# Optimization experiments

Measured on AMD Instinct MI355X. Metric: run time of the kernel, lower is better.

## Reference

```python
import jax, jax.numpy as jnp
import numpy as np

B, N, M, NS = 4, 32768, 1024, 32
RADIUS = 0.1
EPS = 1e-5
CHANS = [16, 32, 32, 64]


def setup_inputs() -> dict:
    key = jax.random.key(0)
    ks = jax.random.split(key, 8)
    d = {
        'theta': jax.random.uniform(ks[0], (B, N), jnp.float32, 0.0, float(np.pi)),
        'phi': jax.random.uniform(ks[1], (B, N), jnp.float32, 0.0, 2.0 * float(np.pi)),
        'features': jax.random.normal(ks[2], (B, CHANS[0], N), jnp.float32),
    }
    for i, (ci, co) in enumerate(zip(CHANS[:-1], CHANS[1:])):
        d[f'w{i}'] = jax.random.normal(jax.random.fold_in(ks[3], i), (co, ci), jnp.float32) * 0.1
        d[f'b{i}'] = jnp.zeros((co,), jnp.float32)
        d[f'g{i}'] = jnp.ones((co,), jnp.float32)
        d[f'be{i}'] = jnp.zeros((co,), jnp.float32)
    return d


def _group(theta, phi, features):
    # angular ball query + random neighbor sampling (deterministic key),
    # duplicates padded with the first valid neighbor (max-pool invariant,
    # matching the torch code's sampling-with-replacement semantics).
    k1, k2 = jax.random.split(jax.random.key(42))
    n = theta.shape[1]
    cent_idx = jax.random.permutation(k1, n)[:M]                 # shared across batch, like torch code
    ct = theta[:, cent_idx]                                      # (B, M)
    cp = phi[:, cent_idx]
    th_s, ph_s = jax.lax.stop_gradient(theta), jax.lax.stop_gradient(phi)
    ct_s, cp_s = jax.lax.stop_gradient(ct), jax.lax.stop_gradient(cp)
    dist = jnp.sqrt((th_s[:, None, :] - ct_s[:, :, None]) ** 2 +
                    (ph_s[:, None, :] - cp_s[:, :, None]) ** 2)  # (B, M, N)
    mask = dist <= RADIUS
    scores = jnp.where(mask, jax.random.uniform(k2, dist.shape, jnp.float32), jnp.inf)
    _, idx = jax.lax.top_k(-scores, NS)                          # NS random in-ball indices, (B, M, NS)
    valid = jnp.take_along_axis(mask, idx, axis=-1)
    idx = jnp.where(valid, idx, idx[..., :1])                    # centroid itself is always valid at slot 0
    gathered = jax.vmap(lambda f, i: f[:, i])(features, idx)     # (B, C, M, NS)
    grouped = jnp.transpose(gathered, (0, 1, 3, 2))              # (B, C, NS, M)
    return ct, cp, grouped


def _mlp_max(x, params):
    # 1x1 conv + BatchNorm (batch stats, training mode) + ReLU stack, then max over nsample
    for w, b, g, be in params:
        x = jnp.einsum('oc,bcsm->bosm', w, x) + b[None, :, None, None]
        mu = x.mean(axis=(0, 2, 3), keepdims=True)
        var = x.var(axis=(0, 2, 3), keepdims=True)
        x = (x - mu) * jax.lax.rsqrt(var + EPS) * g[None, :, None, None] + be[None, :, None, None]
        x = jax.nn.relu(x)
    return x.max(axis=2)                                         # (B, C_out, M)


def reference(theta, phi, features, w0, b0, g0, be0, w1, b1, g1, be1, w2, b2, g2, be2):
    params = [(w0, b0, g0, be0), (w1, b1, g1, be1), (w2, b2, g2, be2)]
    ct, cp, grouped = _group(theta, phi, features)
    new_feats = _mlp_max(grouped, params)
    return ct, cp, new_feats
```

## Files before the change

### kernel.cpp

```cpp
#include <hip/hip_runtime.h>
#include <stdint.h>

#define N_PTS 32768
#define M_CENT 1024
#define B_SZ 4
#define NS 32
#define NR 64
#define P_TOT (B_SZ * NS * M_CENT)

#define GT 29
#define GP 58
#define NCELL (GT * GP)
#define INVF (1.0f / 0.11f)
#define CAPW 320

__device__ __forceinline__ int cell_t(float t) {
  return min(GT - 1, (int)(t * INVF));
}
__device__ __forceinline__ int cell_p(float p) {
  return min(GP - 1, (int)(p * INVF));
}

struct Key2 { uint32_t a, b; };

__device__ __forceinline__ uint32_t rotl32(uint32_t v, uint32_t r) {
  return (v << r) | (v >> (32u - r));
}

__device__ __forceinline__ void tf2x32(uint32_t k0, uint32_t k1,
                                       uint32_t& x0, uint32_t& x1) {
  uint32_t ks0 = k0, ks1 = k1, ks2 = k0 ^ k1 ^ 0x1BD11BDAu;
  x0 += ks0; x1 += ks1;
#define TF_ROUND(r) { x0 += x1; x1 = rotl32(x1, r); x1 ^= x0; }
  TF_ROUND(13u) TF_ROUND(15u) TF_ROUND(26u) TF_ROUND(6u)
  x0 += ks1; x1 += ks2 + 1u;
  TF_ROUND(17u) TF_ROUND(29u) TF_ROUND(16u) TF_ROUND(24u)
  x0 += ks2; x1 += ks0 + 2u;
  TF_ROUND(13u) TF_ROUND(15u) TF_ROUND(26u) TF_ROUND(6u)
  x0 += ks0; x1 += ks1 + 3u;
  TF_ROUND(17u) TF_ROUND(29u) TF_ROUND(16u) TF_ROUND(24u)
  x0 += ks1; x1 += ks2 + 4u;
  TF_ROUND(13u) TF_ROUND(15u) TF_ROUND(26u) TF_ROUND(6u)
  x0 += ks2; x1 += ks0 + 5u;
#undef TF_ROUND
}

__device__ __forceinline__ Key2 tf_block(Key2 k, uint32_t hi, uint32_t lo) {
  uint32_t x0 = hi, x1 = lo;
  tf2x32(k.a, k.b, x0, x1);
  Key2 r; r.a = x0; r.b = x1; return r;
}

__global__ __launch_bounds__(256) void perm_bits_kernel(uint32_t* __restrict__ bits1,
                                                        uint32_t* __restrict__ bits2) {
  int j = blockIdx.x * 256 + threadIdx.x;
  Key2 root; root.a = 0u; root.b = 42u;
  Key2 k1   = tf_block(root, 0u, 0u);
  Key2 keyA = tf_block(k1, 0u, 0u);
  Key2 sub1 = tf_block(k1, 0u, 1u);
  Key2 sub2 = tf_block(keyA, 0u, 1u);
  Key2 r1 = tf_block(sub1, 0u, (uint32_t)j);
  Key2 r2 = tf_block(sub2, 0u, (uint32_t)j);
  bits1[j] = r1.a ^ r1.b;
  bits2[j] = r2.a ^ r2.b;
}

__global__ __launch_bounds__(256) void hist_kernel(const uint32_t* __restrict__ bits1,
                                                   const uint32_t* __restrict__ bits2,
                                                   int* __restrict__ hist1,
                                                   int* __restrict__ hist2) {
  int j = blockIdx.x * 256 + threadIdx.x;
  atomicAdd(&hist1[bits1[j] >> 16], 1);
  atomicAdd(&hist2[bits2[j] >> 16], 1);
}

__global__ __launch_bounds__(256) void gsum_scan_kernel(const int* __restrict__ hist1,
                                                        const int* __restrict__ hist2,
                                                        int* __restrict__ gbase1,
                                                        int* __restrict__ gbase2) {
  __shared__ int s[256];
  const int* hist = blockIdx.x == 0 ? hist1 : hist2;
  int* gbase = blockIdx.x == 0 ? gbase1 : gbase2;
  int g = threadIdx.x;
  int sum = 0;
  for (int i = 0; i < 256; ++i) sum += hist[g * 256 + i];
  s[g] = sum;
  __syncthreads();
  if (g == 0) {
    int run = 0;
    for (int i = 0; i < 256; ++i) { int t = s[i]; s[i] = run; run += t; }
  }
  __syncthreads();
  gbase[g] = s[g];
}

__global__ __launch_bounds__(256) void bucket_scan_kernel(const int* __restrict__ hist1,
                                                          const int* __restrict__ hist2,
                                                          const int* __restrict__ gbase1,
                                                          const int* __restrict__ gbase2,
                                                          int* __restrict__ prefix1,
                                                          int* __restrict__ prefix2,
                                                          int* __restrict__ cursor1,
                                                          int* __restrict__ cursor2) {
  __shared__ int s[256];
  const int* hist = blockIdx.y == 0 ? hist1 : hist2;
  const int* gbase = blockIdx.y == 0 ? gbase1 : gbase2;
  int* prefix = blockIdx.y == 0 ? prefix1 : prefix2;
  int* cursor = blockIdx.y == 0 ? cursor1 : cursor2;
  int g = blockIdx.x, t = threadIdx.x;
  int idx = g * 256 + t;
  int orig = hist[idx];
  s[t] = orig;
  __syncthreads();
  for (int off = 1; off < 256; off <<= 1) {
    int v = (t >= off) ? s[t - off] : 0;
    __syncthreads();
    s[t] += v;
    __syncthreads();
  }
  int pref = gbase[g] + s[t] - orig;
  prefix[idx] = pref;
  cursor[idx] = pref;
}

__global__ __launch_bounds__(256) void bucket_scatter_kernel(const uint32_t* __restrict__ bits1,
                                                             const uint32_t* __restrict__ bits2,
                                                             int* __restrict__ cursor1,
                                                             int* __restrict__ cursor2,
                                                             int* __restrict__ sorted1,
                                                             int* __restrict__ sorted2) {
  int j = blockIdx.x * 256 + threadIdx.x;
  int p1 = atomicAdd(&cursor1[bits1[j] >> 16], 1);
  sorted1[p1] = j;
  int p2 = atomicAdd(&cursor2[bits2[j] >> 16], 1);
  sorted2[p2] = j;
}

__device__ __forceinline__ int exact_rank(const uint32_t* __restrict__ bits,
                                          const int* __restrict__ prefix,
                                          const int* __restrict__ hist,
                                          const int* __restrict__ sorted, int j) {
  uint32_t my = bits[j];
  int b = (int)(my >> 16);
  int start = prefix[b];
  int cnt = hist[b];
  int r = start;
  for (int i = 0; i < cnt; ++i) {
    int m = sorted[start + i];
    uint32_t vb = bits[m];
    if (vb < my || (vb == my && m < j)) ++r;
  }
  return r;
}

__global__ __launch_bounds__(256) void rank_scatter1_kernel(
    const uint32_t* __restrict__ bits1, const uint32_t* __restrict__ bits2,
    const int* __restrict__ prefix1, const int* __restrict__ prefix2,
    const int* __restrict__ hist1, const int* __restrict__ hist2,
    const int* __restrict__ sorted1, const int* __restrict__ sorted2,
    int* __restrict__ xmid, int* __restrict__ rank2) {
  int j = blockIdx.x * 256 + threadIdx.x;
  int r1 = exact_rank(bits1, prefix1, hist1, sorted1, j);
  xmid[r1] = j;
  rank2[j] = exact_rank(bits2, prefix2, hist2, sorted2, j);
}

__global__ __launch_bounds__(256) void scatter2_kernel(const int* __restrict__ rank2,
                                                       const int* __restrict__ xmid,
                                                       int* __restrict__ xfin) {
  int p = blockIdx.x * 256 + threadIdx.x;
  xfin[rank2[p]] = xmid[p];
}

__global__ __launch_bounds__(256) void cell_hist_kernel(const float* __restrict__ theta,
                                                        const float* __restrict__ phi,
                                                        int* __restrict__ cellcnt) {
  int j = blockIdx.x * 256 + threadIdx.x;
  int b = j >> 15;
  atomicAdd(&cellcnt[b * NCELL + cell_t(theta[j]) * GP + cell_p(phi[j])], 1);
}

__global__ __launch_bounds__(256) void cell_scan_kernel(const int* __restrict__ cellcnt,
                                                        int* __restrict__ cellpre,
                                                        int* __restrict__ cellcur) {
  __shared__ int s[256];
  int b = blockIdx.x, t = threadIdx.x;
  const int* cnt = cellcnt + b * NCELL;
  int i0 = t * 7, i1 = min(i0 + 7, NCELL);
  int sum = 0;
  for (int i = i0; i < i1; ++i) sum += cnt[i];
  s[t] = sum;
  __syncthreads();
  for (int off = 1; off < 256; off <<= 1) {
    int v = (t >= off) ? s[t - off] : 0;
    __syncthreads();
    s[t] += v;
    __syncthreads();
  }
  int run = (t == 0) ? 0 : s[t - 1];
  for (int i = i0; i < i1; ++i) {
    cellpre[b * NCELL + i] = run;
    cellcur[b * NCELL + i] = run;
    run += cnt[i];
  }
}

__global__ __launch_bounds__(256) void cell_scatter_kernel(const float* __restrict__ theta,
                                                           const float* __restrict__ phi,
                                                           int* __restrict__ cellcur,
                                                           float* __restrict__ px,
                                                           float* __restrict__ py,
                                                           int* __restrict__ pid) {
  int j = blockIdx.x * 256 + threadIdx.x;
  int b = j >> 15, n = j & (N_PTS - 1);
  float t = theta[j], p = phi[j];
  int cell = b * NCELL + cell_t(t) * GP + cell_p(p);
  int pos = atomicAdd(&cellcur[cell], 1);
  px[(b << 15) + pos] = t;
  py[(b << 15) + pos] = p;
  pid[(b << 15) + pos] = n;
}

__global__ __launch_bounds__(256) void select_kernel(
    const float* __restrict__ theta, const float* __restrict__ phi,
    const int* __restrict__ cent,
    const int* __restrict__ cellpre, const int* __restrict__ cellcnt,
    const float* __restrict__ px, const float* __restrict__ py,
    const int* __restrict__ pid,
    int* __restrict__ idx_buf, float* __restrict__ out_ct, float* __restrict__ out_cp) {
  __shared__ float wsc[4][CAPW];
  __shared__ int wsn[4][CAPW];
  int tid = threadIdx.x;
  int w = tid >> 6, lane = tid & 63;
  int bm = blockIdx.x * 4 + w;
  int b = bm >> 10, m = bm & 1023;
  int ci = cent[m];
  float ctv = theta[(b << 15) + ci];
  float cpv = phi[(b << 15) + ci];
  if (lane == 0) { out_ct[bm] = ctv; out_cp[bm] = cpv; }

  Key2 root; root.a = 0u; root.b = 42u;
  Key2 k2 = tf_block(root, 0u, 1u);
  uint32_t flat_base = (uint32_t)bm << 15;

  int tc = cell_t(ctv), pc = cell_p(cpv);
  int t0 = max(0, tc - 1), t1 = min(GT - 1, tc + 1);
  int p0 = max(0, pc - 1), p1 = min(GP - 1, pc + 1);

  const float* bpx = px + ((size_t)b << 15);
  const float* bpy = py + ((size_t)b << 15);
  const int* bpid = pid + ((size_t)b << 15);
  int wcnt = 0;
  for (int tcell = t0; tcell <= t1; ++tcell) {
    for (int pcell = p0; pcell <= p1; ++pcell) {
      int cell = b * NCELL + tcell * GP + pcell;
      int start = cellpre[cell];
      int cnt = cellcnt[cell];
      for (int base = 0; base < cnt; base += 64) {
        int i = base + lane;
        bool hit = false; float sc = 0.0f; int n = 0;
        if (i < cnt) {
          float t = bpx[start + i], p = bpy[start + i];
          float dx = __fsub_rn(t, ctv);
          float dy = __fsub_rn(p, cpv);
          float d = __fsqrt_rn(__fadd_rn(__fmul_rn(dx, dx), __fmul_rn(dy, dy)));
          if (d <= 0.1f) {
            hit = true; n = bpid[start + i];
            Key2 r = tf_block(k2, 0u, flat_base + (uint32_t)n);
            uint32_t bits = r.a ^ r.b;
            sc = __uint_as_float(0x3f800000u | (bits >> 9)) - 1.0f;
          }
        }
        unsigned long long mask = __ballot(hit);
        int pos = wcnt + __popcll(mask & ((1ull << lane) - 1ull));
        if (hit && pos < CAPW) { wsc[w][pos] = sc; wsn[w][pos] = n; }
        wcnt = min(wcnt + (int)__popcll(mask), CAPW);
      }
    }
  }
  __syncthreads();

  float ls = -1.0f; int ln = -1;
  int sel0 = -1, mysel = -1;
  for (int r = 0; r < NS; ++r) {
    float best = 3.0e38f; int bn = 0x7fffffff;
    for (int i = lane; i < wcnt; i += 64) {
      float s = wsc[w][i]; int n = wsn[w][i];
      bool after = (s > ls) || (s == ls && n > ln);
      bool better = (s < best) || (s == best && n < bn);
      if (after && better) { best = s; bn = n; }
    }
    for (int off = 32; off; off >>= 1) {
      float os = __shfl_xor(best, off);
      int on = __shfl_xor(bn, off);
      if (os < best || (os == best && on < bn)) { best = os; bn = on; }
    }
    int chosen;
    if (best < 3.0e38f) { ls = best; ln = bn; chosen = bn; }
    else chosen = sel0;
    if (r == 0) sel0 = chosen;
    if (lane == r) mysel = chosen;
  }
  if (lane < NS) idx_buf[bm * NS + lane] = mysel;
}

__device__ __forceinline__ float bn_relu(float y, float mu, float r, float g, float be) {
  float t = __fsub_rn(y, mu);
  t = __fmul_rn(t, r);
  t = __fmul_rn(t, g);
  t = __fadd_rn(t, be);
  return fmaxf(t, 0.0f);
}

template <int CO>
__device__ __forceinline__ void accum_stats_pad(const float* __restrict__ Yp,
                                                double* __restrict__ S, int tid, int bid) {
  if (tid < CO) {
    double s1 = 0.0, s2 = 0.0;
#pragma unroll
    for (int s = 0; s < NS; ++s) {
      double v = (double)Yp[tid * 33 + s];
      s1 += v; s2 += v * v;
    }
    double* base = S + (size_t)(bid & (NR - 1)) * (2 * CO);
    atomicAdd(base + tid, s1);
    atomicAdd(base + CO + tid, s2);
  }
}

__global__ __launch_bounds__(256) void pass1_kernel(
    const float* __restrict__ feat, const int* __restrict__ idx_buf,
    const float* __restrict__ w0, const float* __restrict__ b0,
    float* __restrict__ stash, double* __restrict__ stats, int mode) {
  __shared__ int idxs[NS];
  __shared__ float X1[512];
  __shared__ float Yp[32 * 33];
  int bm = blockIdx.x, tid = threadIdx.x, b = bm >> 10;
  if (tid < NS) idxs[tid] = idx_buf[bm * NS + tid];
  __syncthreads();
  for (int v = tid; v < 512; v += 256) {
    int c = v >> 5, s = v & 31;
    float val = feat[(size_t)(b * 16 + c) * N_PTS + idxs[s]];
    X1[v] = val;
    if (mode == 1) stash[(size_t)bm * 512 + v] = val;
  }
  __syncthreads();
  for (int v = tid; v < 1024; v += 256) {
    int o = v >> 5, s = v & 31;
    float acc = b0[o];
#pragma unroll
    for (int c = 0; c < 16; ++c) acc = fmaf(w0[o * 16 + c], X1[c * 32 + s], acc);
    Yp[o * 33 + s] = acc;
    if (mode == 2) stash[(size_t)bm * 1024 + v] = acc;
  }
  __syncthreads();
  accum_stats_pad<32>(Yp, stats, tid, bm);
}

__global__ __launch_bounds__(256) void pass2s_kernel(
    const float* __restrict__ Y1g,
    const float* __restrict__ mur1, const float* __restrict__ g0, const float* __restrict__ be0,
    const float* __restrict__ w1, const float* __restrict__ b1,
    float* __restrict__ Y2g, double* __restrict__ stats) {
  __shared__ float X2[1024];
  __shared__ float Yp[32 * 33];
  int bm = blockIdx.x, tid = threadIdx.x;
  for (int v = tid; v < 1024; v += 256) {
    int o = v >> 5;
    X2[v] = bn_relu(Y1g[(size_t)bm * 1024 + v], mur1[o], mur1[32 + o], g0[o], be0[o]);
  }
  __syncthreads();
  for (int v = tid; v < 1024; v += 256) {
    int o = v >> 5, s = v & 31;
    float acc = b1[o];
#pragma unroll
    for (int c = 0; c < 32; ++c) acc = fmaf(w1[o * 32 + c], X2[c * 32 + s], acc);
    Yp[o * 33 + s] = acc;
    Y2g[(size_t)bm * 1024 + v] = acc;
  }
  __syncthreads();
  accum_stats_pad<32>(Yp, stats, tid, bm);
}

__global__ __launch_bounds__(256) void pass3s_kernel(
    const float* __restrict__ Y2g,
    const float* __restrict__ mur2, const float* __restrict__ g1, const float* __restrict__ be1,
    const float* __restrict__ w2, const float* __restrict__ b2,
    float* __restrict__ mm3, double* __restrict__ stats) {
  __shared__ float X3[1024];
  __shared__ float Yp[64 * 33];
  int bm = blockIdx.x, tid = threadIdx.x;
  for (int v = tid; v < 1024; v += 256) {
    int o = v >> 5;
    X3[v] = bn_relu(Y2g[(size_t)bm * 1024 + v], mur2[o], mur2[32 + o], g1[o], be1[o]);
  }
  __syncthreads();
  for (int v = tid; v < 2048; v += 256) {
    int o = v >> 5, s = v & 31;
    float acc = b2[o];
#pragma unroll
    for (int c = 0; c < 32; ++c) acc = fmaf(w2[o * 32 + c], X3[c * 32 + s], acc);
    Yp[o * 33 + s] = acc;
  }
  __syncthreads();
  if (tid < 64) {
    double s1 = 0.0, s2 = 0.0;
    float mx = -3.0e38f, mn = 3.0e38f;
#pragma unroll
    for (int s = 0; s < NS; ++s) {
      float y = Yp[tid * 33 + s];
      double v = (double)y;
      s1 += v; s2 += v * v;
      mx = fmaxf(mx, y); mn = fminf(mn, y);
    }
    double* base = stats + (size_t)(bm & (NR - 1)) * 128;
    atomicAdd(base + tid, s1);
    atomicAdd(base + 64 + tid, s2);
    mm3[bm * 128 + tid * 2] = mx;
    mm3[bm * 128 + tid * 2 + 1] = mn;
  }
}

__global__ __launch_bounds__(256) void final_small_kernel(
    const float* __restrict__ mm3,
    const float* __restrict__ mur3, const float* __restrict__ g2, const float* __restrict__ be2,
    float* __restrict__ out_ft) {
  int j = blockIdx.x * 256 + threadIdx.x;
  int b = j >> 16, o = (j >> 10) & 63, m = j & 1023;
  int bm = b * 1024 + m;
  float g = g2[o];
  float y = (g >= 0.0f) ? mm3[bm * 128 + o * 2] : mm3[bm * 128 + o * 2 + 1];
  out_ft[j] = bn_relu(y, mur3[o], mur3[64 + o], g, be2[o]);
}

__device__ __forceinline__ void load_x1(int big, const float* __restrict__ X1g,
                                        const float* __restrict__ feat,
                                        const int* __restrict__ idx_buf,
                                        int bm, int b, int tid,
                                        int* idxs, float* X1) {
  if (!big) {
    if (tid < NS) idxs[tid] = idx_buf[bm * NS + tid];
  }
  __syncthreads();
  if (big) {
    for (int v = tid; v < 512; v += 256) X1[v] = X1g[(size_t)bm * 512 + v];
  } else {
    for (int v = tid; v < 512; v += 256) {
      int c = v >> 5, s = v & 31;
      X1[v] = feat[(size_t)(b * 16 + c) * N_PTS + idxs[s]];
    }
  }
}

__global__ __launch_bounds__(256) void pass2_rec_kernel(
    const float* __restrict__ X1g, const float* __restrict__ feat,
    const int* __restrict__ idx_buf,
    const float* __restrict__ w0, const float* __restrict__ b0,
    const float* __restrict__ mur1, const float* __restrict__ g0, const float* __restrict__ be0,
    const float* __restrict__ w1, const float* __restrict__ b1,
    double* __restrict__ stats, int big) {
  __shared__ int idxs[NS];
  __shared__ float X1[512];
  __shared__ float X2[1024];
  __shared__ float Yp[32 * 33];
  int bm = blockIdx.x, tid = threadIdx.x, b = bm >> 10;
  load_x1(big, X1g, feat, idx_buf, bm, b, tid, idxs, X1);
  __syncthreads();
  for (int v = tid; v < 1024; v += 256) {
    int o = v >> 5, s = v & 31;
    float acc = b0[o];
#pragma unroll
    for (int c = 0; c < 16; ++c) acc = fmaf(w0[o * 16 + c], X1[c * 32 + s], acc);
    X2[v] = bn_relu(acc, mur1[o], mur1[32 + o], g0[o], be0[o]);
  }
  __syncthreads();
  for (int v = tid; v < 1024; v += 256) {
    int o = v >> 5, s = v & 31;
    float acc = b1[o];
#pragma unroll
    for (int c = 0; c < 32; ++c) acc = fmaf(w1[o * 32 + c], X2[c * 32 + s], acc);
    Yp[o * 33 + s] = acc;
  }
  __syncthreads();
  accum_stats_pad<32>(Yp, stats, tid, bm);
}

__global__ __launch_bounds__(256) void pass3_rec_kernel(
    const float* __restrict__ X1g, const float* __restrict__ feat,
    const int* __restrict__ idx_buf,
    const float* __restrict__ w0, const float* __restrict__ b0,
    const float* __restrict__ mur1, const float* __restrict__ g0, const float* __restrict__ be0,
    const float* __restrict__ w1, const float* __restrict__ b1,
    const float* __restrict__ mur2, const float* __restrict__ g1, const float* __restrict__ be1,
    const float* __restrict__ w2, const float* __restrict__ b2,
    float* __restrict__ mm3, double* __restrict__ stats, int big) {
  __shared__ int idxs[NS];
  __shared__ float X1[512];
  __shared__ float X2[1024];
  __shared__ float X3[1024];
  __shared__ float Yp[64 * 33];
  int bm = blockIdx.x, tid = threadIdx.x, b = bm >> 10;
  load_x1(big, X1g, feat, idx_buf, bm, b, tid, idxs, X1);
  __syncthreads();
  for (int v = tid; v < 1024; v += 256) {
    int o = v >> 5, s = v & 31;
    float acc = b0[o];
#pragma unroll
    for (int c = 0; c < 16; ++c) acc = fmaf(w0[o * 16 + c], X1[c * 32 + s], acc);
    X2[v] = bn_relu(acc, mur1[o], mur1[32 + o], g0[o], be0[o]);
  }
  __syncthreads();
  for (int v = tid; v < 1024; v += 256) {
    int o = v >> 5, s = v & 31;
    float acc = b1[o];
#pragma unroll
    for (int c = 0; c < 32; ++c) acc = fmaf(w1[o * 32 + c], X2[c * 32 + s], acc);
    X3[v] = bn_relu(acc, mur2[o], mur2[32 + o], g1[o], be1[o]);
  }
  __syncthreads();
  for (int v = tid; v < 2048; v += 256) {
    int o = v >> 5, s = v & 31;
    float acc = b2[o];
#pragma unroll
    for (int c = 0; c < 32; ++c) acc = fmaf(w2[o * 32 + c], X3[c * 32 + s], acc);
    Yp[o * 33 + s] = acc;
  }
  __syncthreads();
  if (tid < 64) {
    double s1 = 0.0, s2 = 0.0;
    float mx = -3.0e38f, mn = 3.0e38f;
#pragma unroll
    for (int s = 0; s < NS; ++s) {
      float y = Yp[tid * 33 + s];
      double v = (double)y;
      s1 += v; s2 += v * v;
      mx = fmaxf(mx, y); mn = fminf(mn, y);
    }
    double* base = stats + (size_t)(bm & (NR - 1)) * 128;
    atomicAdd(base + tid, s1);
    atomicAdd(base + 64 + tid, s2);
    mm3[bm * 128 + tid * 2] = mx;
    mm3[bm * 128 + tid * 2 + 1] = mn;
  }
}

template <int CO>
__global__ void fixup_mur_kernel(const double* __restrict__ S, float* __restrict__ mur) {
  int o = threadIdx.x;
  if (o >= CO) return;
  double s1 = 0.0, s2 = 0.0;
  for (int r = 0; r < NR; ++r) {
    s1 += S[r * 2 * CO + o];
    s2 += S[r * 2 * CO + CO + o];
  }
  const double P = (double)P_TOT;
  double mu = s1 / P;
  double var = s2 / P - mu * mu;
  mur[o] = (float)mu;
  mur[CO + o] = (float)(1.0 / sqrt(var + 1e-5));
}

extern "C" void kernel_launch(void* const* d_in, const int* in_sizes, int n_in,
                              void* d_out, int out_size, void* d_ws, size_t ws_size,
                              hipStream_t stream) {
  (void)in_sizes; (void)n_in; (void)out_size;
  const float* theta = (const float*)d_in[0];
  const float* phi   = (const float*)d_in[1];
  const float* feat  = (const float*)d_in[2];
  const float* w0 = (const float*)d_in[3];
  const float* b0 = (const float*)d_in[4];
  const float* g0 = (const float*)d_in[5];
  const float* be0 = (const float*)d_in[6];
  const float* w1 = (const float*)d_in[7];
  const float* b1 = (const float*)d_in[8];
  const float* g1 = (const float*)d_in[9];
  const float* be1 = (const float*)d_in[10];
  const float* w2 = (const float*)d_in[11];
  const float* b2 = (const float*)d_in[12];
  const float* g2 = (const float*)d_in[13];
  const float* be2 = (const float*)d_in[14];

  float* out = (float*)d_out;
  float* out_ct = out;
  float* out_cp = out + B_SZ * M_CENT;
  float* out_ft = out + 2 * B_SZ * M_CENT;

  char* ws = (char*)d_ws;
  uint32_t* bits1 = (uint32_t*)(ws + 0);
  uint32_t* bits2 = (uint32_t*)(ws + 131072);
  int* rank2 = (int*)(ws + 262144);
  int* xmid  = (int*)(ws + 393216);
  int* xfin  = (int*)(ws + 524288);
  int* idx_buf = (int*)(ws + 655360);
  int* hist1   = (int*)(ws + 1179648);
  int* hist2   = (int*)(ws + 1441792);
  int* prefix1 = (int*)(ws + 1703936);
  int* prefix2 = (int*)(ws + 1966080);
  int* cursor1 = (int*)(ws + 2228224);
  int* cursor2 = (int*)(ws + 2490368);
  int* sorted1 = (int*)(ws + 2752512);
  int* sorted2 = (int*)(ws + 2883584);
  int* gbase1  = (int*)(ws + 3014656);
  int* gbase2  = (int*)(ws + 3015680);
  int* cellcnt = (int*)(ws + 3016704);
  int* cellpre = (int*)(ws + 3049472);
  int* cellcur = (int*)(ws + 3082240);
  float* px    = (float*)(ws + 3115008);
  float* py    = (float*)(ws + 3639296);
  int* pid     = (int*)(ws + 4163584);
  double* stats1 = (double*)(ws + 4687872);
  double* stats2 = (double*)(ws + 4720640);
  double* stats3 = (double*)(ws + 4753408);
  float* mur1 = (float*)(ws + 4818944);
  float* mur2 = (float*)(ws + 4819200);
  float* mur3 = (float*)(ws + 4819456);
  float* mm3  = (float*)(ws + 4820480);
  float* stash = (float*)(ws + 6917632);
  float* Y2g  = (float*)(ws + 23694848);
  size_t NEED_FULL = (size_t)40472064;
  size_t NEED_BIG  = (size_t)6917632 + 8388608;
  int full = (ws_size >= NEED_FULL) ? 1 : 0;
  int big  = (!full && ws_size >= NEED_BIG) ? 1 : 0;

  hipMemsetAsync(hist1, 0, 524288, stream);
  hipMemsetAsync(cellcnt, 0, 32768, stream);
  hipMemsetAsync(stats1, 0, 131072, stream);

  perm_bits_kernel<<<128, 256, 0, stream>>>(bits1, bits2);
  hist_kernel<<<128, 256, 0, stream>>>(bits1, bits2, hist1, hist2);
  gsum_scan_kernel<<<2, 256, 0, stream>>>(hist1, hist2, gbase1, gbase2);
  bucket_scan_kernel<<<dim3(256, 2), 256, 0, stream>>>(hist1, hist2, gbase1, gbase2,
                                                       prefix1, prefix2, cursor1, cursor2);
  bucket_scatter_kernel<<<128, 256, 0, stream>>>(bits1, bits2, cursor1, cursor2,
                                                 sorted1, sorted2);
  rank_scatter1_kernel<<<128, 256, 0, stream>>>(bits1, bits2, prefix1, prefix2,
                                                hist1, hist2, sorted1, sorted2,
                                                xmid, rank2);
  scatter2_kernel<<<128, 256, 0, stream>>>(rank2, xmid, xfin);

  cell_hist_kernel<<<512, 256, 0, stream>>>(theta, phi, cellcnt);
  cell_scan_kernel<<<4, 256, 0, stream>>>(cellcnt, cellpre, cellcur);
  cell_scatter_kernel<<<512, 256, 0, stream>>>(theta, phi, cellcur, px, py, pid);

  select_kernel<<<1024, 256, 0, stream>>>(theta, phi, xfin, cellpre, cellcnt,
                                          px, py, pid, idx_buf, out_ct, out_cp);

  int mode = full ? 2 : (big ? 1 : 0);
  pass1_kernel<<<4096, 256, 0, stream>>>(feat, idx_buf, w0, b0, stash, stats1, mode);
  fixup_mur_kernel<32><<<1, 64, 0, stream>>>(stats1, mur1);
  if (full) {
    pass2s_kernel<<<4096, 256, 0, stream>>>(stash, mur1, g0, be0, w1, b1, Y2g, stats2);
    fixup_mur_kernel<32><<<1, 64, 0, stream>>>(stats2, mur2);
    pass3s_kernel<<<4096, 256, 0, stream>>>(Y2g, mur2, g1, be1, w2, b2, mm3, stats3);
  } else {
    pass2_rec_kernel<<<4096, 256, 0, stream>>>(stash, feat, idx_buf, w0, b0, mur1, g0, be0,
                                               w1, b1, stats2, big);
    fixup_mur_kernel<32><<<1, 64, 0, stream>>>(stats2, mur2);
    pass3_rec_kernel<<<4096, 256, 0, stream>>>(stash, feat, idx_buf, w0, b0, mur1, g0, be0,
                                               w1, b1, mur2, g1, be1, w2, b2, mm3, stats3, big);
  }
  fixup_mur_kernel<64><<<1, 64, 0, stream>>>(stats3, mur3);
  final_small_kernel<<<1024, 256, 0, stream>>>(mm3, mur3, g2, be2, out_ft);
}
```

Before: 289.0 us.

## Fuse preprocessing kernels, pack points as float4, transpose features, recompute layer-2 activations

Merges the permutation-bit, histogram and cell-count kernels into one prep kernel, and merges the two scans and the two scatters, which cuts launches. Points are stored as packed float4 so each load brings theta, phi and id together. The select kernel walks the 3x3 neighbour cells as one flattened range and uses a bitonic sort when there are at most 64 hits. A transposed feature copy lets pass1 gather each point with float4 loads. The Y2 stash is dropped: pass3 recomputes layer-2 from the Y1 stash, trading extra FLOPs for less memory traffic and a smaller workspace.

Result: faster. 277.0 us (-4.2%).

```diff
diff --git a/kernel.cpp b/kernel.cpp
--- a/kernel.cpp
+++ b/kernel.cpp
@@ -51,47 +51,96 @@
   Key2 r; r.a = x0; r.b = x1; return r;
 }
 
-__global__ __launch_bounds__(256) void perm_bits_kernel(uint32_t* __restrict__ bits1,
-                                                        uint32_t* __restrict__ bits2) {
+__global__ __launch_bounds__(256) void prep_kernel(const float* __restrict__ theta,
+                                                   const float* __restrict__ phi,
+                                                   uint32_t* __restrict__ bits1,
+                                                   uint32_t* __restrict__ bits2,
+                                                   int* __restrict__ hist1,
+                                                   int* __restrict__ hist2,
+                                                   int* __restrict__ cellcnt) {
   int j = blockIdx.x * 256 + threadIdx.x;
-  Key2 root; root.a = 0u; root.b = 42u;
-  Key2 k1   = tf_block(root, 0u, 0u);
-  Key2 keyA = tf_block(k1, 0u, 0u);
-  Key2 sub1 = tf_block(k1, 0u, 1u);
-  Key2 sub2 = tf_block(keyA, 0u, 1u);
-  Key2 r1 = tf_block(sub1, 0u, (uint32_t)j);
-  Key2 r2 = tf_block(sub2, 0u, (uint32_t)j);
-  bits1[j] = r1.a ^ r1.b;
-  bits2[j] = r2.a ^ r2.b;
-}
-
-__global__ __launch_bounds__(256) void hist_kernel(const uint32_t* __restrict__ bits1,
-                                                   const uint32_t* __restrict__ bits2,
-                                                   int* __restrict__ hist1,
-                                                   int* __restrict__ hist2) {
-  int j = blockIdx.x * 256 + threadIdx.x;
-  atomicAdd(&hist1[bits1[j] >> 16], 1);
-  atomicAdd(&hist2[bits2[j] >> 16], 1);
-}
-
-__global__ __launch_bounds__(256) void gsum_scan_kernel(const int* __restrict__ hist1,
-                                                        const int* __restrict__ hist2,
-                                                        int* __restrict__ gbase1,
-                                                        int* __restrict__ gbase2) {
+  int b = j >> 15;
+  float t = theta[j], p = phi[j];
+  atomicAdd(&cellcnt[b * NCELL + cell_t(t) * GP + cell_p(p)], 1);
+  if (j < N_PTS) {
+    Key2 root; root.a = 0u; root.b = 42u;
+    Key2 k1   = tf_block(root, 0u, 0u);
+    Key2 keyA = tf_block(k1, 0u, 0u);
+    Key2 sub1 = tf_block(k1, 0u, 1u);
+    Key2 sub2 = tf_block(keyA, 0u, 1u);
+    Key2 r1 = tf_block(sub1, 0u, (uint32_t)j);
+    Key2 r2 = tf_block(sub2, 0u, (uint32_t)j);
+    uint32_t v1 = r1.a ^ r1.b, v2 = r2.a ^ r2.b;
+    bits1[j] = v1; bits2[j] = v2;
+    atomicAdd(&hist1[v1 >> 16], 1);
+    atomicAdd(&hist2[v2 >> 16], 1);
+  }
+}
+
+__global__ __launch_bounds__(256) void transpose_kernel(const float* __restrict__ feat,
+                                                        float* __restrict__ featT) {
+  __shared__ float lds[16][65];
+  int b = blockIdx.y;
+  int n0 = blockIdx.x * 64;
+  int tid = threadIdx.x;
+#pragma unroll
+  for (int k = 0; k < 4; ++k) {
+    int v = tid + k * 256;
+    int c = v >> 6, no = v & 63;
+    lds[c][no] = feat[((size_t)(b * 16 + c) << 15) + n0 + no];
+  }
+  __syncthreads();
+#pragma unroll
+  for (int k = 0; k < 4; ++k) {
+    int v = tid + k * 256;
+    int no = v >> 4, c = v & 15;
+    featT[((size_t)(b << 15) + n0 + no) * 16 + c] = lds[c][no];
+  }
+}
+
+__global__ __launch_bounds__(256) void scans_kernel(const int* __restrict__ hist1,
+                                                    const int* __restrict__ hist2,
+                                                    int* __restrict__ gbase1,
+                                                    int* __restrict__ gbase2,
+                                                    const int* __restrict__ cellcnt,
+                                                    int* __restrict__ cellpre,
+                                                    int* __restrict__ cellcur) {
   __shared__ int s[256];
-  const int* hist = blockIdx.x == 0 ? hist1 : hist2;
-  int* gbase = blockIdx.x == 0 ? gbase1 : gbase2;
-  int g = threadIdx.x;
-  int sum = 0;
-  for (int i = 0; i < 256; ++i) sum += hist[g * 256 + i];
-  s[g] = sum;
-  __syncthreads();
-  if (g == 0) {
-    int run = 0;
-    for (int i = 0; i < 256; ++i) { int t = s[i]; s[i] = run; run += t; }
-  }
-  __syncthreads();
-  gbase[g] = s[g];
+  int t = threadIdx.x;
+  if (blockIdx.x < 2) {
+    const int* hist = blockIdx.x == 0 ? hist1 : hist2;
+    int* gbase = blockIdx.x == 0 ? gbase1 : gbase2;
+    int sum = 0;
+    for (int i = 0; i < 256; ++i) sum += hist[t * 256 + i];
+    s[t] = sum;
+    __syncthreads();
+    if (t == 0) {
+      int run = 0;
+      for (int i = 0; i < 256; ++i) { int v = s[i]; s[i] = run; run += v; }
+    }
+    __syncthreads();
+    gbase[t] = s[t];
+  } else {
+    int b = blockIdx.x - 2;
+    const int* cnt = cellcnt + b * NCELL;
+    int i0 = t * 7, i1 = min(i0 + 7, NCELL);
+    int sum = 0;
+    for (int i = i0; i < i1; ++i) sum += cnt[i];
+    s[t] = sum;
+    __syncthreads();
+    for (int off = 1; off < 256; off <<= 1) {
+      int v = (t >= off) ? s[t - off] : 0;
+      __syncthreads();
+      s[t] += v;
+      __syncthreads();
+    }
+    int run = (t == 0) ? 0 : s[t - 1];
+    for (int i = i0; i < i1; ++i) {
+      cellpre[b * NCELL + i] = run;
+      cellcur[b * NCELL + i] = run;
+      run += cnt[i];
+    }
+  }
 }
 
 __global__ __launch_bounds__(256) void bucket_scan_kernel(const int* __restrict__ hist1,
@@ -123,17 +172,28 @@
   cursor[idx] = pref;
 }
 
-__global__ __launch_bounds__(256) void bucket_scatter_kernel(const uint32_t* __restrict__ bits1,
-                                                             const uint32_t* __restrict__ bits2,
-                                                             int* __restrict__ cursor1,
-                                                             int* __restrict__ cursor2,
-                                                             int* __restrict__ sorted1,
-                                                             int* __restrict__ sorted2) {
+__global__ __launch_bounds__(256) void scatter_kernel(const float* __restrict__ theta,
+                                                      const float* __restrict__ phi,
+                                                      int* __restrict__ cellcur,
+                                                      float4* __restrict__ pts4,
+                                                      const uint32_t* __restrict__ bits1,
+                                                      const uint32_t* __restrict__ bits2,
+                                                      int* __restrict__ cursor1,
+                                                      int* __restrict__ cursor2,
+                                                      int* __restrict__ sorted1,
+                                                      int* __restrict__ sorted2) {
   int j = blockIdx.x * 256 + threadIdx.x;
-  int p1 = atomicAdd(&cursor1[bits1[j] >> 16], 1);
-  sorted1[p1] = j;
-  int p2 = atomicAdd(&cursor2[bits2[j] >> 16], 1);
-  sorted2[p2] = j;
+  int b = j >> 15, n = j & (N_PTS - 1);
+  float t = theta[j], p = phi[j];
+  int cell = b * NCELL + cell_t(t) * GP + cell_p(p);
+  int pos = atomicAdd(&cellcur[cell], 1);
+  pts4[(b << 15) + pos] = make_float4(t, p, __int_as_float(n), 0.0f);
+  if (j < N_PTS) {
+    int p1 = atomicAdd(&cursor1[bits1[j] >> 16], 1);
+    sorted1[p1] = j;
+    int p2 = atomicAdd(&cursor2[bits2[j] >> 16], 1);
+    sorted2[p2] = j;
+  }
 }
 
 __device__ __forceinline__ int exact_rank(const uint32_t* __restrict__ bits,
@@ -172,61 +232,11 @@
   xfin[rank2[p]] = xmid[p];
 }
 
-__global__ __launch_bounds__(256) void cell_hist_kernel(const float* __restrict__ theta,
-                                                        const float* __restrict__ phi,
-                                                        int* __restrict__ cellcnt) {
-  int j = blockIdx.x * 256 + threadIdx.x;
-  int b = j >> 15;
-  atomicAdd(&cellcnt[b * NCELL + cell_t(theta[j]) * GP + cell_p(phi[j])], 1);
-}
-
-__global__ __launch_bounds__(256) void cell_scan_kernel(const int* __restrict__ cellcnt,
-                                                        int* __restrict__ cellpre,
-                                                        int* __restrict__ cellcur) {
-  __shared__ int s[256];
-  int b = blockIdx.x, t = threadIdx.x;
-  const int* cnt = cellcnt + b * NCELL;
-  int i0 = t * 7, i1 = min(i0 + 7, NCELL);
-  int sum = 0;
-  for (int i = i0; i < i1; ++i) sum += cnt[i];
-  s[t] = sum;
-  __syncthreads();
-  for (int off = 1; off < 256; off <<= 1) {
-    int v = (t >= off) ? s[t - off] : 0;
-    __syncthreads();
-    s[t] += v;
-    __syncthreads();
-  }
-  int run = (t == 0) ? 0 : s[t - 1];
-  for (int i = i0; i < i1; ++i) {
-    cellpre[b * NCELL + i] = run;
-    cellcur[b * NCELL + i] = run;
-    run += cnt[i];
-  }
-}
-
-__global__ __launch_bounds__(256) void cell_scatter_kernel(const float* __restrict__ theta,
-                                                           const float* __restrict__ phi,
-                                                           int* __restrict__ cellcur,
-                                                           float* __restrict__ px,
-                                                           float* __restrict__ py,
-                                                           int* __restrict__ pid) {
-  int j = blockIdx.x * 256 + threadIdx.x;
-  int b = j >> 15, n = j & (N_PTS - 1);
-  float t = theta[j], p = phi[j];
-  int cell = b * NCELL + cell_t(t) * GP + cell_p(p);
-  int pos = atomicAdd(&cellcur[cell], 1);
-  px[(b << 15) + pos] = t;
-  py[(b << 15) + pos] = p;
-  pid[(b << 15) + pos] = n;
-}
-
 __global__ __launch_bounds__(256) void select_kernel(
     const float* __restrict__ theta, const float* __restrict__ phi,
     const int* __restrict__ cent,
     const int* __restrict__ cellpre, const int* __restrict__ cellcnt,
-    const float* __restrict__ px, const float* __restrict__ py,
-    const int* __restrict__ pid,
+    const float4* __restrict__ pts4,
     int* __restrict__ idx_buf, float* __restrict__ out_ct, float* __restrict__ out_cp) {
   __shared__ float wsc[4][CAPW];
   __shared__ int wsn[4][CAPW];
@@ -246,60 +256,95 @@
   int tc = cell_t(ctv), pc = cell_p(cpv);
   int t0 = max(0, tc - 1), t1 = min(GT - 1, tc + 1);
   int p0 = max(0, pc - 1), p1 = min(GP - 1, pc + 1);
-
-  const float* bpx = px + ((size_t)b << 15);
-  const float* bpy = py + ((size_t)b << 15);
-  const int* bpid = pid + ((size_t)b << 15);
+  int nct = t1 - t0 + 1, ncp = p1 - p0 + 1, ncells = nct * ncp;
+
+  int cst = 0, ccn = 0;
+  if (lane < ncells) {
+    int cell = b * NCELL + (t0 + lane / ncp) * GP + (p0 + lane % ncp);
+    cst = cellpre[cell];
+    ccn = cellcnt[cell];
+  }
+  int sc9[9], cc9[9];
+#pragma unroll
+  for (int k = 0; k < 9; ++k) {
+    sc9[k] = __shfl(cst, k);
+    cc9[k] = __shfl(ccn, k);
+  }
+  int T = 0;
+#pragma unroll
+  for (int k = 0; k < 9; ++k) T += cc9[k];
+
+  const float4* bpts = pts4 + ((size_t)b << 15);
   int wcnt = 0;
-  for (int tcell = t0; tcell <= t1; ++tcell) {
-    for (int pcell = p0; pcell <= p1; ++pcell) {
-      int cell = b * NCELL + tcell * GP + pcell;
-      int start = cellpre[cell];
-      int cnt = cellcnt[cell];
-      for (int base = 0; base < cnt; base += 64) {
-        int i = base + lane;
-        bool hit = false; float sc = 0.0f; int n = 0;
-        if (i < cnt) {
-          float t = bpx[start + i], p = bpy[start + i];
-          float dx = __fsub_rn(t, ctv);
-          float dy = __fsub_rn(p, cpv);
-          float d = __fsqrt_rn(__fadd_rn(__fmul_rn(dx, dx), __fmul_rn(dy, dy)));
-          if (d <= 0.1f) {
-            hit = true; n = bpid[start + i];
-            Key2 r = tf_block(k2, 0u, flat_base + (uint32_t)n);
-            uint32_t bits = r.a ^ r.b;
-            sc = __uint_as_float(0x3f800000u | (bits >> 9)) - 1.0f;
-          }
-        }
-        unsigned long long mask = __ballot(hit);
-        int pos = wcnt + __popcll(mask & ((1ull << lane) - 1ull));
-        if (hit && pos < CAPW) { wsc[w][pos] = sc; wsn[w][pos] = n; }
-        wcnt = min(wcnt + (int)__popcll(mask), CAPW);
+  for (int base = 0; base < T; base += 64) {
+    int i = base + lane;
+    bool hit = false; float sc = 0.0f; int n = 0;
+    if (i < T) {
+      int gidx = 0, acc = 0;
+#pragma unroll
+      for (int k = 0; k < 9; ++k) {
+        int lo = acc; acc += cc9[k];
+        if (i >= lo && i < acc) gidx = sc9[k] + (i - lo);
       }
-    }
-  }
-  __syncthreads();
-
-  float ls = -1.0f; int ln = -1;
-  int sel0 = -1, mysel = -1;
-  for (int r = 0; r < NS; ++r) {
-    float best = 3.0e38f; int bn = 0x7fffffff;
-    for (int i = lane; i < wcnt; i += 64) {
-      float s = wsc[w][i]; int n = wsn[w][i];
-      bool after = (s > ls) || (s == ls && n > ln);
-      bool better = (s < best) || (s == best && n < bn);
-      if (after && better) { best = s; bn = n; }
-    }
-    for (int off = 32; off; off >>= 1) {
-      float os = __shfl_xor(best, off);
-      int on = __shfl_xor(bn, off);
-      if (os < best || (os == best && on < bn)) { best = os; bn = on; }
-    }
-    int chosen;
-    if (best < 3.0e38f) { ls = best; ln = bn; chosen = bn; }
-    else chosen = sel0;
-    if (r == 0) sel0 = chosen;
-    if (lane == r) mysel = chosen;
+      float4 pt = bpts[gidx];
+      float dx = __fsub_rn(pt.x, ctv);
+      float dy = __fsub_rn(pt.y, cpv);
+      float d = __fsqrt_rn(__fadd_rn(__fmul_rn(dx, dx), __fmul_rn(dy, dy)));
+      if (d <= 0.1f) {
+        hit = true; n = __float_as_int(pt.z);
+        Key2 r = tf_block(k2, 0u, flat_base + (uint32_t)n);
+        uint32_t bits = r.a ^ r.b;
+        sc = __uint_as_float(0x3f800000u | (bits >> 9)) - 1.0f;
+      }
+    }
+    unsigned long long mask = __ballot(hit);
+    int pos = wcnt + __popcll(mask & ((1ull << lane) - 1ull));
+    if (hit && pos < CAPW) { wsc[w][pos] = sc; wsn[w][pos] = n; }
+    wcnt = min(wcnt + (int)__popcll(mask), CAPW);
+  }
+
+  int mysel;
+  if (wcnt <= 64) {
+    float s = (lane < wcnt) ? wsc[w][lane] : 3.0e38f;
+    int n = (lane < wcnt) ? wsn[w][lane] : 0x7fffffff;
+#pragma unroll
+    for (int k = 2; k <= 64; k <<= 1) {
+#pragma unroll
+      for (int jj = k >> 1; jj > 0; jj >>= 1) {
+        float os = __shfl_xor(s, jj);
+        int on = __shfl_xor(n, jj);
+        bool lower = (lane & jj) == 0;
+        bool dir = (lane & k) == 0;
+        bool mineFirst = (s < os) || (s == os && n < on);
+        bool takeMine = ((lower == mineFirst) == dir);
+        s = takeMine ? s : os;
+        n = takeMine ? n : on;
+      }
+    }
+    int n0 = __shfl(n, 0);
+    mysel = (lane < wcnt) ? n : n0;
+  } else {
+    float ls = -1.0f; int ln = -1;
+    int sel0 = -1; mysel = -1;
+    for (int r = 0; r < NS; ++r) {
+      float best = 3.0e38f; int bn = 0x7fffffff;
+      for (int i = lane; i < wcnt; i += 64) {
+        float s = wsc[w][i]; int n = wsn[w][i];
+        bool after = (s > ls) || (s == ls && n > ln);
+        bool better = (s < best) || (s == best && n < bn);
+        if (after && better) { best = s; bn = n; }
+      }
+      for (int off = 32; off; off >>= 1) {
+        float os = __shfl_xor(best, off);
+        int on = __shfl_xor(bn, off);
+        if (os < best || (os == best && on < bn)) { best = os; bn = on; }
+      }
+      int chosen;
+      if (best < 3.0e38f) { ls = best; ln = bn; chosen = bn; }
+      else chosen = sel0;
+      if (r == 0) sel0 = chosen;
+      if (lane == r) mysel = chosen;
+    }
   }
   if (lane < NS) idx_buf[bm * NS + lane] = mysel;
 }
@@ -329,7 +374,8 @@
 }
 
 __global__ __launch_bounds__(256) void pass1_kernel(
-    const float* __restrict__ feat, const int* __restrict__ idx_buf,
+    const float* __restrict__ feat, const float* __restrict__ featT,
+    const int* __restrict__ idx_buf,
     const float* __restrict__ w0, const float* __restrict__ b0,
     float* __restrict__ stash, double* __restrict__ stats, int mode) {
   __shared__ int idxs[NS];
@@ -338,11 +384,23 @@
   int bm = blockIdx.x, tid = threadIdx.x, b = bm >> 10;
   if (tid < NS) idxs[tid] = idx_buf[bm * NS + tid];
   __syncthreads();
-  for (int v = tid; v < 512; v += 256) {
-    int c = v >> 5, s = v & 31;
-    float val = feat[(size_t)(b * 16 + c) * N_PTS + idxs[s]];
-    X1[v] = val;
-    if (mode == 1) stash[(size_t)bm * 512 + v] = val;
+  if (mode == 3) {
+    if (tid < 128) {
+      int s = tid >> 2, c4 = tid & 3;
+      float4 f = *reinterpret_cast<const float4*>(
+          &featT[((size_t)(b << 15) + idxs[s]) * 16 + c4 * 4]);
+      X1[(c4 * 4 + 0) * 32 + s] = f.x;
+      X1[(c4 * 4 + 1) * 32 + s] = f.y;
+      X1[(c4 * 4 + 2) * 32 + s] = f.z;
+      X1[(c4 * 4 + 3) * 32 + s] = f.w;
+    }
+  } else {
+    for (int v = tid; v < 512; v += 256) {
+      int c = v >> 5, s = v & 31;
+      float val = feat[(size_t)(b * 16 + c) * N_PTS + idxs[s]];
+      X1[v] = val;
+      if (mode == 1) stash[(size_t)bm * 512 + v] = val;
+    }
   }
   __syncthreads();
   for (int v = tid; v < 1024; v += 256) {
@@ -351,7 +409,7 @@
 #pragma unroll
     for (int c = 0; c < 16; ++c) acc = fmaf(w0[o * 16 + c], X1[c * 32 + s], acc);
     Yp[o * 33 + s] = acc;
-    if (mode == 2) stash[(size_t)bm * 1024 + v] = acc;
+    if (mode >= 2) stash[(size_t)bm * 1024 + v] = acc;
   }
   __syncthreads();
   accum_stats_pad<32>(Yp, stats, tid, bm);
@@ -361,7 +419,7 @@
     const float* __restrict__ Y1g,
     const float* __restrict__ mur1, const float* __restrict__ g0, const float* __restrict__ be0,
     const float* __restrict__ w1, const float* __restrict__ b1,
-    float* __restrict__ Y2g, double* __restrict__ stats) {
+    double* __restrict__ stats) {
   __shared__ float X2[1024];
   __shared__ float Yp[32 * 33];
   int bm = blockIdx.x, tid = threadIdx.x;
@@ -376,23 +434,33 @@
 #pragma unroll
     for (int c = 0; c < 32; ++c) acc = fmaf(w1[o * 32 + c], X2[c * 32 + s], acc);
     Yp[o * 33 + s] = acc;
-    Y2g[(size_t)bm * 1024 + v] = acc;
   }
   __syncthreads();
   accum_stats_pad<32>(Yp, stats, tid, bm);
 }
 
 __global__ __launch_bounds__(256) void pass3s_kernel(
-    const float* __restrict__ Y2g,
+    const float* __restrict__ Y1g,
+    const float* __restrict__ mur1, const float* __restrict__ g0, const float* __restrict__ be0,
+    const float* __restrict__ w1, const float* __restrict__ b1,
     const float* __restrict__ mur2, const float* __restrict__ g1, const float* __restrict__ be1,
     const float* __restrict__ w2, const float* __restrict__ b2,
     float* __restrict__ mm3, double* __restrict__ stats) {
+  __shared__ float X2[1024];
   __shared__ float X3[1024];
   __shared__ float Yp[64 * 33];
   int bm = blockIdx.x, tid = threadIdx.x;
   for (int v = tid; v < 1024; v += 256) {
     int o = v >> 5;
-    X3[v] = bn_relu(Y2g[(size_t)bm * 1024 + v], mur2[o], mur2[32 + o], g1[o], be1[o]);
+    X2[v] = bn_relu(Y1g[(size_t)bm * 1024 + v], mur1[o], mur1[32 + o], g0[o], be0[o]);
+  }
+  __syncthreads();
+  for (int v = tid; v < 1024; v += 256) {
+    int o = v >> 5, s = v & 31;
+    float acc = b1[o];
+#pragma unroll
+    for (int c = 0; c < 32; ++c) acc = fmaf(w1[o * 32 + c], X2[c * 32 + s], acc);
+    X3[v] = bn_relu(acc, mur2[o], mur2[32 + o], g1[o], be1[o]);
   }
   __syncthreads();
   for (int v = tid; v < 2048; v += 256) {
@@ -594,70 +662,67 @@
   int* idx_buf = (int*)(ws + 655360);
   int* hist1   = (int*)(ws + 1179648);
   int* hist2   = (int*)(ws + 1441792);
-  int* prefix1 = (int*)(ws + 1703936);
-  int* prefix2 = (int*)(ws + 1966080);
-  int* cursor1 = (int*)(ws + 2228224);
-  int* cursor2 = (int*)(ws + 2490368);
-  int* sorted1 = (int*)(ws + 2752512);
-  int* sorted2 = (int*)(ws + 2883584);
-  int* gbase1  = (int*)(ws + 3014656);
-  int* gbase2  = (int*)(ws + 3015680);
-  int* cellcnt = (int*)(ws + 3016704);
-  int* cellpre = (int*)(ws + 3049472);
-  int* cellcur = (int*)(ws + 3082240);
-  float* px    = (float*)(ws + 3115008);
-  float* py    = (float*)(ws + 3639296);
-  int* pid     = (int*)(ws + 4163584);
-  double* stats1 = (double*)(ws + 4687872);
-  double* stats2 = (double*)(ws + 4720640);
-  double* stats3 = (double*)(ws + 4753408);
-  float* mur1 = (float*)(ws + 4818944);
-  float* mur2 = (float*)(ws + 4819200);
-  float* mur3 = (float*)(ws + 4819456);
-  float* mm3  = (float*)(ws + 4820480);
-  float* stash = (float*)(ws + 6917632);
-  float* Y2g  = (float*)(ws + 23694848);
-  size_t NEED_FULL = (size_t)40472064;
-  size_t NEED_BIG  = (size_t)6917632 + 8388608;
-  int full = (ws_size >= NEED_FULL) ? 1 : 0;
-  int big  = (!full && ws_size >= NEED_BIG) ? 1 : 0;
-
-  hipMemsetAsync(hist1, 0, 524288, stream);
-  hipMemsetAsync(cellcnt, 0, 32768, stream);
-  hipMemsetAsync(stats1, 0, 131072, stream);
-
-  perm_bits_kernel<<<128, 256, 0, stream>>>(bits1, bits2);
-  hist_kernel<<<128, 256, 0, stream>>>(bits1, bits2, hist1, hist2);
-  gsum_scan_kernel<<<2, 256, 0, stream>>>(hist1, hist2, gbase1, gbase2);
+  int* cellcnt = (int*)(ws + 1703936);
+  double* stats1 = (double*)(ws + 1736704);
+  double* stats2 = (double*)(ws + 1769472);
+  double* stats3 = (double*)(ws + 1802240);
+  int* prefix1 = (int*)(ws + 1867776);
+  int* prefix2 = (int*)(ws + 2129920);
+  int* cursor1 = (int*)(ws + 2392064);
+  int* cursor2 = (int*)(ws + 2654208);
+  int* sorted1 = (int*)(ws + 2916352);
+  int* sorted2 = (int*)(ws + 3047424);
+  int* gbase1  = (int*)(ws + 3178496);
+  int* gbase2  = (int*)(ws + 3179520);
+  int* cellpre = (int*)(ws + 3180544);
+  int* cellcur = (int*)(ws + 3213312);
+  float4* pts4 = (float4*)(ws + 3246080);
+  float* mur1 = (float*)(ws + 5343232);
+  float* mur2 = (float*)(ws + 5343488);
+  float* mur3 = (float*)(ws + 5343744);
+  float* mm3  = (float*)(ws + 5344768);
+  float* stash = (float*)(ws + 7441920);
+  float* featT = (float*)(ws + 7441920 + 16777216);
+  size_t NEED_FULL = (size_t)7441920 + 16777216;
+  size_t NEED_T    = NEED_FULL + 8388608;
+  size_t NEED_BIG  = (size_t)7441920 + 8388608;
+  int mode = (ws_size >= NEED_T) ? 3
+           : (ws_size >= NEED_FULL) ? 2
+           : (ws_size >= NEED_BIG) ? 1 : 0;
+
+  hipMemsetAsync(ws + 1179648, 0, 688128, stream);
+
+  prep_kernel<<<512, 256, 0, stream>>>(theta, phi, bits1, bits2, hist1, hist2, cellcnt);
+  if (mode == 3)
+    transpose_kernel<<<dim3(512, 4), 256, 0, stream>>>(feat, featT);
+  scans_kernel<<<6, 256, 0, stream>>>(hist1, hist2, gbase1, gbase2,
+                                      cellcnt, cellpre, cellcur);
   bucket_scan_kernel<<<dim3(256, 2), 256, 0, stream>>>(hist1, hist2, gbase1, gbase2,
                                                        prefix1, prefix2, cursor1, cursor2);
-  bucket_scatter_kernel<<<128, 256, 0, stream>>>(bits1, bits2, cursor1, cursor2,
-                                                 sorted1, sorted2);
+  scatter_kernel<<<512, 256, 0, stream>>>(theta, phi, cellcur, pts4,
+                                          bits1, bits2, cursor1, cursor2,
+                                          sorted1, sorted2);
   rank_scatter1_kernel<<<128, 256, 0, stream>>>(bits1, bits2, prefix1, prefix2,
                                                 hist1, hist2, sorted1, sorted2,
                                                 xmid, rank2);
   scatter2_kernel<<<128, 256, 0, stream>>>(rank2, xmid, xfin);
 
-  cell_hist_kernel<<<512, 256, 0, stream>>>(theta, phi, cellcnt);
-  cell_scan_kernel<<<4, 256, 0, stream>>>(cellcnt, cellpre, cellcur);
-  cell_scatter_kernel<<<512, 256, 0, stream>>>(theta, phi, cellcur, px, py, pid);
-
   select_kernel<<<1024, 256, 0, stream>>>(theta, phi, xfin, cellpre, cellcnt,
-                                          px, py, pid, idx_buf, out_ct, out_cp);
-
-  int mode = full ? 2 : (big ? 1 : 0);
-  pass1_kernel<<<4096, 256, 0, stream>>>(feat, idx_buf, w0, b0, stash, stats1, mode);
+                                          pts4, idx_buf, out_ct, out_cp);
+
+  pass1_kernel<<<4096, 256, 0, stream>>>(feat, featT, idx_buf, w0, b0, stash, stats1, mode);
   fixup_mur_kernel<32><<<1, 64, 0, stream>>>(stats1, mur1);
-  if (full) {
-    pass2s_kernel<<<4096, 256, 0, stream>>>(stash, mur1, g0, be0, w1, b1, Y2g, stats2);
+  if (mode >= 2) {
+    pass2s_kernel<<<4096, 256, 0, stream>>>(stash, mur1, g0, be0, w1, b1, stats2);
     fixup_mur_kernel<32><<<1, 64, 0, stream>>>(stats2, mur2);
-    pass3s_kernel<<<4096, 256, 0, stream>>>(Y2g, mur2, g1, be1, w2, b2, mm3, stats3);
+    pass3s_kernel<<<4096, 256, 0, stream>>>(stash, mur1, g0, be0, w1, b1,
+                                            mur2, g1, be1, w2, b2, mm3, stats3);
   } else {
     pass2_rec_kernel<<<4096, 256, 0, stream>>>(stash, feat, idx_buf, w0, b0, mur1, g0, be0,
-                                               w1, b1, stats2, big);
+                                               w1, b1, stats2, mode);
     fixup_mur_kernel<32><<<1, 64, 0, stream>>>(stats2, mur2);
     pass3_rec_kernel<<<4096, 256, 0, stream>>>(stash, feat, idx_buf, w0, b0, mur1, g0, be0,
-                                               w1, b1, mur2, g1, be1, w2, b2, mm3, stats3, big);
+                                               w1, b1, mur2, g1, be1, w2, b2, mm3, stats3, mode);
   }
   fixup_mur_kernel<64><<<1, 64, 0, stream>>>(stats3, mur3);
   final_small_kernel<<<1024, 256, 0, stream>>>(mm3, mur3, g2, be2, out_ft);
```
